# Optimization experiments

Hardware: AMD Instinct MI355X
Metric: run time of the kernel (lower is better)

## Reference

```python
import jax, jax.numpy as jnp
import numpy as np

B, D, NQ, NL, OUT = 256, 512, 16, 4, 10
NSTATES = 2 ** NQ
C64 = jnp.complex64


def _rx(t):
    c = jnp.cos(t / 2).astype(C64)
    s = (-1j * jnp.sin(t / 2)).astype(C64)
    return jnp.stack([jnp.stack([c, s], -1), jnp.stack([s, c], -1)], -2)


def _ry(t):
    c = jnp.cos(t / 2).astype(C64)
    s = jnp.sin(t / 2).astype(C64)
    return jnp.stack([jnp.stack([c, -s], -1), jnp.stack([s, c], -1)], -2)


def _rz(t):
    em = jnp.exp(-0.5j * t.astype(jnp.float32)).astype(C64)
    ep = jnp.exp(0.5j * t.astype(jnp.float32)).astype(C64)
    z = jnp.zeros_like(em)
    return jnp.stack([jnp.stack([em, z], -1), jnp.stack([z, ep], -1)], -2)


def _apply_gate(state, U, q, n):
    # state: (B, 2^n); U: (2,2) shared or (B,2,2) per-sample; qubit q is MSB-first
    b = state.shape[0]
    st = state.reshape(b, 2 ** q, 2, 2 ** (n - q - 1))
    if U.ndim == 2:
        st = jnp.einsum('ij,bajc->baic', U, st)
    else:
        st = jnp.einsum('bij,bajc->baic', U, st)
    return st.reshape(b, -1)


def _signs_table(n):
    # signs[i, q] = +-1 spin of qubit q (MSB-first) in basis state i
    idx = np.arange(2 ** n, dtype=np.int64)
    bits = (idx[:, None] >> (n - 1 - np.arange(n))[None, :]) & 1
    return jnp.asarray(1.0 - 2.0 * bits, dtype=jnp.float32)


def setup_inputs() -> dict:
    key = jax.random.key(0)
    ks = jax.random.split(key, 8)
    return {
        'x': jax.random.normal(ks[0], (B, D), dtype=jnp.float32),
        'W_enc': jax.random.normal(ks[1], (D, NQ), dtype=jnp.float32) * 0.05,
        'b_enc': jnp.zeros((NQ,), dtype=jnp.float32),
        'theta': jax.random.normal(ks[2], (NL, NQ, 3), dtype=jnp.float32) * 0.1,
        'phi': jax.random.normal(ks[3], (NL, NQ), dtype=jnp.float32) * 0.1,
        'W1': jax.random.normal(ks[4], (NQ, 2 * NQ), dtype=jnp.float32) * 0.1,
        'b1': jnp.zeros((2 * NQ,), dtype=jnp.float32),
        'W2': jax.random.normal(ks[5], (2 * NQ, OUT), dtype=jnp.float32) * 0.1,
        'b2': jnp.zeros((OUT,), dtype=jnp.float32),
    }


def reference(x, W_enc, b_enc, theta, phi, W1, b1, W2, b2):
    n, L = NQ, NL
    signs = _signs_table(n)                      # (2^n, n)
    zz = signs * jnp.roll(signs, -1, axis=1)     # ring ZZ couplings (2^n, n)

    # 1) classical -> angle encoding
    angles = jnp.tanh(x @ W_enc + b_enc) * jnp.pi          # (B, n)

    # 2) statevector init |0...0>
    state = jnp.zeros((x.shape[0], NSTATES), dtype=C64).at[:, 0].set(1.0)

    # 3) per-sample RY encoding layer
    for q in range(n):
        state = _apply_gate(state, _ry(angles[:, q]), q, n)

    # 4) variational layers: RZ->RY->RX per qubit, then entangling ZZ ring (diagonal)
    for l in range(L):
        for q in range(n):
            U = _rx(theta[l, q, 0]) @ _ry(theta[l, q, 1]) @ _rz(theta[l, q, 2])
            state = _apply_gate(state, U, q, n)
        phase = jnp.exp(-0.5j * (zz @ phi[l]))             # (2^n,)
        state = state * phase[None, :].astype(C64)

    # 5) <Z_q> expectation values
    probs = jnp.abs(state) ** 2                            # (B, 2^n)
    z = probs @ signs                                      # (B, n)

    # 6) classical decoder (dropout inactive at eval)
    h = jax.nn.relu(z @ W1 + b1)
    return h @ W2 + b2
```

## Files before the change

kernel.cpp:

```cpp
#include <hip/hip_runtime.h>


struct c32 { float x, y; };

__device__ __forceinline__ c32 cmul(c32 a, c32 b) {
  return { a.x * b.x - a.y * b.y, a.x * b.y + a.y * b.x };
}
__device__ __forceinline__ c32 C32(float2 f) { return { f.x, f.y }; }
__device__ __forceinline__ float2 F2(c32 a) { return make_float2(a.x, a.y); }
__device__ __forceinline__ c32 csel(c32 a, c32 b, int s) {
  return { s ? b.x : a.x, s ? b.y : a.y };
}

__device__ __forceinline__ void gate2(c32 &a0, c32 &a1, const c32 u[4]) {
  c32 b0 = a0, b1 = a1;
  a0.x = u[0].x * b0.x - u[0].y * b0.y + u[1].x * b1.x - u[1].y * b1.y;
  a0.y = u[0].x * b0.y + u[0].y * b0.x + u[1].x * b1.y + u[1].y * b1.x;
  a1.x = u[2].x * b0.x - u[2].y * b0.y + u[3].x * b1.x - u[3].y * b1.y;
  a1.y = u[2].x * b0.y + u[2].y * b0.x + u[3].x * b1.y + u[3].y * b1.x;
}

template <int ST>
__device__ __forceinline__ void rgate(c32 *a, const c32 u[4]) {
#pragma unroll
  for (int p = 0; p < 4; p++) {
    int i0 = ((p & ~(ST - 1)) << 1) | (p & (ST - 1));
    gate2(a[i0], a[i0 + ST], u);
  }
}

__device__ __forceinline__ void xgate(c32 *a, const c32 u[4], int lb, int lane) {
  int hi = (lane >> lb) & 1;
  c32 ua = csel(u[0], u[3], hi);
  c32 ub = csel(u[1], u[2], hi);
  int mask = 1 << lb;
#pragma unroll
  for (int r = 0; r < 8; r++) {
    float px = __shfl_xor(a[r].x, mask, 64);
    float py = __shfl_xor(a[r].y, mask, 64);
    c32 o = a[r];
    a[r].x = ua.x * o.x - ua.y * o.y + ub.x * px - ub.y * py;
    a[r].y = ua.x * o.y + ua.y * o.x + ub.x * py + ub.y * px;
  }
}

__device__ __forceinline__ void loadU(const float2* __restrict__ Ug, int idx, c32 u[4]) {
#pragma unroll
  for (int k = 0; k < 4; k++) u[k] = C32(Ug[idx * 4 + k]);
}

__device__ __forceinline__ void make_u(float t0, float t1, float t2, c32 u[4]) {
  float cx = cosf(0.5f * t0), sx = sinf(0.5f * t0);
  float cy = cosf(0.5f * t1), sy = sinf(0.5f * t1);
  float cz = cosf(0.5f * t2), sz = sinf(0.5f * t2);
  c32 M00 = {  cx * cy, -sx * sy };
  c32 M01 = { -cx * sy, -sx * cy };
  c32 M10 = {  cx * sy, -sx * cy };
  c32 M11 = {  cx * cy,  sx * sy };
  c32 em = { cz, -sz }, ep = { cz, sz };
  u[0] = cmul(M00, em);
  u[1] = cmul(M01, ep);
  u[2] = cmul(M10, em);
  u[3] = cmul(M11, ep);
}


__global__ __launch_bounds__(256) void k_prep(const float* __restrict__ x,
                                              const float* __restrict__ W,
                                              const float* __restrict__ be,
                                              const float* __restrict__ theta,
                                              const float* __restrict__ phi,
                                              float2* __restrict__ vtab,
                                              float2* __restrict__ Ug,
                                              float2* __restrict__ qph) {
  int t = threadIdx.x;
  if (blockIdx.x < 256) {
    int b = blockIdx.x;
    int q = t & 15, part = t >> 4;
    const float* xr = x + b * 512;
    float s = 0.f;
#pragma unroll 8
    for (int k = 0; k < 32; k++) {
      int d = part * 32 + k;
      s += xr[d] * W[d * 16 + q];
    }
    __shared__ float red[256];
    red[part * 16 + q] = s;
    __syncthreads();
    for (int st = 8; st > 0; st >>= 1) {
      if (part < st) red[part * 16 + q] += red[(part + st) * 16 + q];
      __syncthreads();
    }
    if (t < 16) {
      float a = tanhf(red[t] + be[t]) * 3.14159265358979323846f;
      float ca = cosf(0.5f * a), sa = sinf(0.5f * a);
      c32 u[4];
      make_u(theta[t * 3 + 0], theta[t * 3 + 1], theta[t * 3 + 2], u);
      vtab[b * 32 + t * 2]     = make_float2(u[0].x * ca + u[1].x * sa,
                                             u[0].y * ca + u[1].y * sa);
      vtab[b * 32 + t * 2 + 1] = make_float2(u[2].x * ca + u[3].x * sa,
                                             u[2].y * ca + u[3].y * sa);
    }
  } else {
    int idx = (blockIdx.x - 256) * 256 + t;
    if (idx < 48) {
      int l = idx >> 4, qq = idx & 15;
      const float* th = theta + ((l + 1) * 16 + qq) * 3;
      c32 u[4];
      make_u(th[0], th[1], th[2], u);
#pragma unroll
      for (int k = 0; k < 4; k++) Ug[idx * 4 + k] = F2(u[k]);
    }
    int q = idx >> 11, l = (idx >> 9) & 3, i = idx & 511;
    float A = 0.f;
    for (int m = l + 1; m <= 8 - l; m++) {
      int j = (q + 4 - m) & 15;
      float wv = phi[l * 16 + j];
      int sg = ((i >> m) ^ (i >> (m - 1))) & 1;
      A += sg ? -wv : wv;
    }
    qph[idx] = make_float2(cosf(0.5f * A), -sinf(0.5f * A));
  }
}


__global__ __launch_bounds__(1024) void k_cone_decode(const float2* __restrict__ vtab,
                                                      const float2* __restrict__ Ug,
                                                      const float2* __restrict__ qph,
                                                      const float* __restrict__ W1,
                                                      const float* __restrict__ b1,
                                                      const float* __restrict__ W2,
                                                      const float* __restrict__ b2,
                                                      float* __restrict__ out) {
  int b = blockIdx.x;
  int tid = threadIdx.x;
  int q = tid >> 6, lane = tid & 63;

  c32 vv0[9], vv1[9];
  const float2* vt = vtab + b * 32;
#pragma unroll
  for (int m = 0; m < 9; m++) {
    int jj = (q + 4 - m) & 15;
    vv0[m] = C32(vt[jj * 2]);
    vv1[m] = C32(vt[jj * 2 + 1]);
  }

  c32 lp = csel(vv0[0], vv1[0], lane & 1);
  lp = cmul(lp, csel(vv0[1], vv1[1], (lane >> 1) & 1));
  lp = cmul(lp, csel(vv0[2], vv1[2], (lane >> 2) & 1));
  lp = cmul(lp, csel(vv0[6], vv1[6], (lane >> 3) & 1));
  lp = cmul(lp, csel(vv0[7], vv1[7], (lane >> 4) & 1));
  lp = cmul(lp, csel(vv0[8], vv1[8], (lane >> 5) & 1));

  c32 a[8];
#pragma unroll
  for (int r = 0; r < 8; r++) {
    c32 tt = cmul(((r & 1) ? vv1[3] : vv0[3]), (((r >> 1) & 1) ? vv1[4] : vv0[4]));
    tt = cmul(tt, (((r >> 2) & 1) ? vv1[5] : vv0[5]));
    a[r] = cmul(lp, tt);
  }

  const float2* ph = qph + q * 2048;
  int ibase = (lane & 7) | (((lane >> 3) & 7) << 6);

  c32 u[4];
#pragma unroll
  for (int r = 0; r < 8; r++) a[r] = cmul(a[r], C32(ph[ibase | (r << 3)]));
  loadU(Ug, 0 * 16 + ((q + 3) & 15), u); xgate(a, u, 1, lane);
  loadU(Ug, 0 * 16 + ((q + 2) & 15), u); xgate(a, u, 2, lane);
  loadU(Ug, 0 * 16 + ((q + 1) & 15), u); rgate<1>(a, u);
  loadU(Ug, 0 * 16 + ( q          ), u); rgate<2>(a, u);
  loadU(Ug, 0 * 16 + ((q - 1) & 15), u); rgate<4>(a, u);
  loadU(Ug, 0 * 16 + ((q - 2) & 15), u); xgate(a, u, 3, lane);
  loadU(Ug, 0 * 16 + ((q - 3) & 15), u); xgate(a, u, 4, lane);
#pragma unroll
  for (int r = 0; r < 8; r++) a[r] = cmul(a[r], C32(ph[512 | ibase | (r << 3)]));
  loadU(Ug, 1 * 16 + ((q + 2) & 15), u); xgate(a, u, 2, lane);
  loadU(Ug, 1 * 16 + ((q + 1) & 15), u); rgate<1>(a, u);
  loadU(Ug, 1 * 16 + ( q          ), u); rgate<2>(a, u);
  loadU(Ug, 1 * 16 + ((q - 1) & 15), u); rgate<4>(a, u);
  loadU(Ug, 1 * 16 + ((q - 2) & 15), u); xgate(a, u, 3, lane);
#pragma unroll
  for (int r = 0; r < 8; r++) a[r] = cmul(a[r], C32(ph[1024 | ibase | (r << 3)]));
  loadU(Ug, 2 * 16 + ((q + 1) & 15), u); rgate<1>(a, u);
  loadU(Ug, 2 * 16 + ( q          ), u); rgate<2>(a, u);
  loadU(Ug, 2 * 16 + ((q - 1) & 15), u); rgate<4>(a, u);
#pragma unroll
  for (int r = 0; r < 8; r++) a[r] = cmul(a[r], C32(ph[1536 | ibase | (r << 3)]));

  float z = 0.f;
#pragma unroll
  for (int r = 0; r < 8; r++) {
    float p = a[r].x * a[r].x + a[r].y * a[r].y;
    z += ((r >> 1) & 1) ? -p : p;
  }
#pragma unroll
  for (int off = 32; off > 0; off >>= 1) z += __shfl_xor(z, off, 64);

  __shared__ float zsh[16];
  __shared__ float hsh[32];
  if (lane == 0) zsh[q] = z;
  __syncthreads();
  if (tid < 32) {
    float hj = b1[tid];
#pragma unroll
    for (int qq = 0; qq < 16; qq++) hj += zsh[qq] * W1[qq * 32 + tid];
    hsh[tid] = fmaxf(hj, 0.f);
  }
  __syncthreads();
  if (tid < 10) {
    float o = b2[tid];
#pragma unroll
    for (int j = 0; j < 32; j++) o += hsh[j] * W2[j * 10 + tid];
    out[b * 10 + tid] = o;
  }
}


extern "C" void kernel_launch(void* const* d_in, const int* in_sizes, int n_in,
                              void* d_out, int out_size, void* d_ws, size_t ws_size,
                              hipStream_t stream) {
  const float* x     = (const float*)d_in[0];
  const float* Wenc  = (const float*)d_in[1];
  const float* benc  = (const float*)d_in[2];
  const float* theta = (const float*)d_in[3];
  const float* phi   = (const float*)d_in[4];
  const float* W1    = (const float*)d_in[5];
  const float* b1    = (const float*)d_in[6];
  const float* W2    = (const float*)d_in[7];
  const float* b2    = (const float*)d_in[8];
  float* out = (float*)d_out;

  char* w = (char*)d_ws;
  float2* vtab  = (float2*)(w);
  float2* Ugtab = (float2*)(w + 65536);
  float2* qph   = (float2*)(w + 69632);

  k_prep<<<384, 256, 0, stream>>>(x, Wenc, benc, theta, phi, vtab, Ugtab, qph);
  k_cone_decode<<<256, 1024, 0, stream>>>(vtab, Ugtab, qph, W1, b1, W2, b2, out);
}
```

Measured before the change: 83.31 us.

## Fuse prep and cone kernels into one, compute ZZ phases inline

Merges the encoder/prep kernel into the light-cone simulation kernel so each block computes its own encoding angles, gate matrices (into shared memory), and halved phi values, removing one launch and the global workspace round trip. The precomputed phase table is replaced by computing ZZ phase sums per amplitude from lane bits and using fast __cosf/__sinf. The cost is that each block redundantly rebuilds the 48 shared gate matrices and does extra trig per amplitude, and fast trig reduces accuracy slightly.

```diff
diff --git a/kernel.cpp b/kernel.cpp
--- a/kernel.cpp
+++ b/kernel.cpp
@@ -11,6 +11,7 @@
 __device__ __forceinline__ c32 csel(c32 a, c32 b, int s) {
   return { s ? b.x : a.x, s ? b.y : a.y };
 }
+__device__ __forceinline__ float fsgn(int s, float w) { return s ? -w : w; }
 
 __device__ __forceinline__ void gate2(c32 &a0, c32 &a1, const c32 u[4]) {
   c32 b0 = a0, b1 = a1;
@@ -44,7 +45,7 @@
   }
 }
 
-__device__ __forceinline__ void loadU(const float2* __restrict__ Ug, int idx, c32 u[4]) {
+__device__ __forceinline__ void loadU(const float2* Ug, int idx, c32 u[4]) {
 #pragma unroll
   for (int k = 0; k < 4; k++) u[k] = C32(Ug[idx * 4 + k]);
 }
@@ -64,93 +65,96 @@
   u[3] = cmul(M11, ep);
 }
 
-
-__global__ __launch_bounds__(256) void k_prep(const float* __restrict__ x,
+__device__ __forceinline__ void diag8(c32 *a, float L, float w3p, float w4,
+                                      float w5, float w6p) {
+#pragma unroll
+  for (int r = 0; r < 8; r++) {
+    int r0 = r & 1, r1 = (r >> 1) & 1, r2 = (r >> 2) & 1;
+    float A = L + (r0 ? -w3p : w3p) + ((r1 ^ r0) ? -w4 : w4)
+                + ((r2 ^ r1) ? -w5 : w5) + (r2 ? -w6p : w6p);
+    c32 p = { __cosf(A), -__sinf(A) };
+    a[r] = cmul(a[r], p);
+  }
+}
+
+
+__global__ __launch_bounds__(1024) void k_all(const float* __restrict__ x,
                                               const float* __restrict__ W,
                                               const float* __restrict__ be,
                                               const float* __restrict__ theta,
                                               const float* __restrict__ phi,
-                                              float2* __restrict__ vtab,
-                                              float2* __restrict__ Ug,
-                                              float2* __restrict__ qph) {
-  int t = threadIdx.x;
-  if (blockIdx.x < 256) {
-    int b = blockIdx.x;
-    int q = t & 15, part = t >> 4;
-    const float* xr = x + b * 512;
+                                              const float* __restrict__ W1,
+                                              const float* __restrict__ b1,
+                                              const float* __restrict__ W2,
+                                              const float* __restrict__ b2,
+                                              float* __restrict__ out) {
+  __shared__ float  red[256];
+  __shared__ float2 vsh[32];
+  __shared__ float2 ugsh[192];
+  __shared__ float  phish[64];
+  __shared__ float  zsh[16];
+  __shared__ float  hsh[32];
+
+  int tid = threadIdx.x, b = blockIdx.x;
+  int lane = tid & 63, wv = tid >> 6;
+
+  {
+    int q16 = tid & 15, part = tid >> 4;
+    const float* xr = x + (b << 9);
     float s = 0.f;
-#pragma unroll 8
-    for (int k = 0; k < 32; k++) {
-      int d = part * 32 + k;
-      s += xr[d] * W[d * 16 + q];
+#pragma unroll
+    for (int k = 0; k < 8; k++) {
+      int d = (part << 3) + k;
+      s += xr[d] * W[(d << 4) + q16];
     }
-    __shared__ float red[256];
-    red[part * 16 + q] = s;
-    __syncthreads();
-    for (int st = 8; st > 0; st >>= 1) {
-      if (part < st) red[part * 16 + q] += red[(part + st) * 16 + q];
-      __syncthreads();
-    }
-    if (t < 16) {
-      float a = tanhf(red[t] + be[t]) * 3.14159265358979323846f;
-      float ca = cosf(0.5f * a), sa = sinf(0.5f * a);
-      c32 u[4];
-      make_u(theta[t * 3 + 0], theta[t * 3 + 1], theta[t * 3 + 2], u);
-      vtab[b * 32 + t * 2]     = make_float2(u[0].x * ca + u[1].x * sa,
-                                             u[0].y * ca + u[1].y * sa);
-      vtab[b * 32 + t * 2 + 1] = make_float2(u[2].x * ca + u[3].x * sa,
-                                             u[2].y * ca + u[3].y * sa);
-    }
-  } else {
-    int idx = (blockIdx.x - 256) * 256 + t;
-    if (idx < 48) {
-      int l = idx >> 4, qq = idx & 15;
-      const float* th = theta + ((l + 1) * 16 + qq) * 3;
-      c32 u[4];
-      make_u(th[0], th[1], th[2], u);
-#pragma unroll
-      for (int k = 0; k < 4; k++) Ug[idx * 4 + k] = F2(u[k]);
-    }
-    int q = idx >> 11, l = (idx >> 9) & 3, i = idx & 511;
-    float A = 0.f;
-    for (int m = l + 1; m <= 8 - l; m++) {
-      int j = (q + 4 - m) & 15;
-      float wv = phi[l * 16 + j];
-      int sg = ((i >> m) ^ (i >> (m - 1))) & 1;
-      A += sg ? -wv : wv;
-    }
-    qph[idx] = make_float2(cosf(0.5f * A), -sinf(0.5f * A));
-  }
-}
-
-
-__global__ __launch_bounds__(1024) void k_cone_decode(const float2* __restrict__ vtab,
-                                                      const float2* __restrict__ Ug,
-                                                      const float2* __restrict__ qph,
-                                                      const float* __restrict__ W1,
-                                                      const float* __restrict__ b1,
-                                                      const float* __restrict__ W2,
-                                                      const float* __restrict__ b2,
-                                                      float* __restrict__ out) {
-  int b = blockIdx.x;
-  int tid = threadIdx.x;
-  int q = tid >> 6, lane = tid & 63;
+    s += __shfl_xor(s, 16, 64);
+    s += __shfl_xor(s, 32, 64);
+    if (lane < 16) red[wv * 16 + lane] = s;
+  }
+  if (tid >= 960 && tid < 1008) {
+    int gl = tid - 960, l = gl >> 4, qq = gl & 15;
+    const float* th = theta + (((l + 1) << 4) + qq) * 3;
+    c32 u[4];
+    make_u(th[0], th[1], th[2], u);
+#pragma unroll
+    for (int k = 0; k < 4; k++) ugsh[gl * 4 + k] = F2(u[k]);
+  } else if (tid >= 896 && tid < 960) {
+    phish[tid - 896] = 0.5f * phi[tid - 896];
+  }
+  __syncthreads();
+  if (tid < 16) {
+    float acc = 0.f;
+#pragma unroll
+    for (int w = 0; w < 16; w++) acc += red[w * 16 + tid];
+    float a = tanhf(acc + be[tid]) * 3.14159265358979323846f;
+    float ca = __cosf(0.5f * a), sa = __sinf(0.5f * a);
+    c32 u[4];
+    make_u(theta[tid * 3 + 0], theta[tid * 3 + 1], theta[tid * 3 + 2], u);
+    vsh[tid * 2]     = make_float2(u[0].x * ca + u[1].x * sa,
+                                   u[0].y * ca + u[1].y * sa);
+    vsh[tid * 2 + 1] = make_float2(u[2].x * ca + u[3].x * sa,
+                                   u[2].y * ca + u[3].y * sa);
+  }
+  __syncthreads();
+
+  int q = wv;
+  int lb0 = lane & 1, lb1 = (lane >> 1) & 1, lb2 = (lane >> 2) & 1;
+  int lb3 = (lane >> 3) & 1, lb4 = (lane >> 4) & 1, lb5 = (lane >> 5) & 1;
 
   c32 vv0[9], vv1[9];
-  const float2* vt = vtab + b * 32;
 #pragma unroll
   for (int m = 0; m < 9; m++) {
     int jj = (q + 4 - m) & 15;
-    vv0[m] = C32(vt[jj * 2]);
-    vv1[m] = C32(vt[jj * 2 + 1]);
-  }
-
-  c32 lp = csel(vv0[0], vv1[0], lane & 1);
-  lp = cmul(lp, csel(vv0[1], vv1[1], (lane >> 1) & 1));
-  lp = cmul(lp, csel(vv0[2], vv1[2], (lane >> 2) & 1));
-  lp = cmul(lp, csel(vv0[6], vv1[6], (lane >> 3) & 1));
-  lp = cmul(lp, csel(vv0[7], vv1[7], (lane >> 4) & 1));
-  lp = cmul(lp, csel(vv0[8], vv1[8], (lane >> 5) & 1));
+    vv0[m] = C32(vsh[jj * 2]);
+    vv1[m] = C32(vsh[jj * 2 + 1]);
+  }
+
+  c32 lp = csel(vv0[0], vv1[0], lb0);
+  lp = cmul(lp, csel(vv0[1], vv1[1], lb1));
+  lp = cmul(lp, csel(vv0[2], vv1[2], lb2));
+  lp = cmul(lp, csel(vv0[6], vv1[6], lb3));
+  lp = cmul(lp, csel(vv0[7], vv1[7], lb4));
+  lp = cmul(lp, csel(vv0[8], vv1[8], lb5));
 
   c32 a[8];
 #pragma unroll
@@ -160,33 +164,34 @@
     a[r] = cmul(lp, tt);
   }
 
-  const float2* ph = qph + q * 2048;
-  int ibase = (lane & 7) | (((lane >> 3) & 7) << 6);
+#define PHW(l, m) phish[(l) * 16 + ((q + 4 - (m)) & 15)]
 
   c32 u[4];
-#pragma unroll
-  for (int r = 0; r < 8; r++) a[r] = cmul(a[r], C32(ph[ibase | (r << 3)]));
-  loadU(Ug, 0 * 16 + ((q + 3) & 15), u); xgate(a, u, 1, lane);
-  loadU(Ug, 0 * 16 + ((q + 2) & 15), u); xgate(a, u, 2, lane);
-  loadU(Ug, 0 * 16 + ((q + 1) & 15), u); rgate<1>(a, u);
-  loadU(Ug, 0 * 16 + ( q          ), u); rgate<2>(a, u);
-  loadU(Ug, 0 * 16 + ((q - 1) & 15), u); rgate<4>(a, u);
-  loadU(Ug, 0 * 16 + ((q - 2) & 15), u); xgate(a, u, 3, lane);
-  loadU(Ug, 0 * 16 + ((q - 3) & 15), u); xgate(a, u, 4, lane);
-#pragma unroll
-  for (int r = 0; r < 8; r++) a[r] = cmul(a[r], C32(ph[512 | ibase | (r << 3)]));
-  loadU(Ug, 1 * 16 + ((q + 2) & 15), u); xgate(a, u, 2, lane);
-  loadU(Ug, 1 * 16 + ((q + 1) & 15), u); rgate<1>(a, u);
-  loadU(Ug, 1 * 16 + ( q          ), u); rgate<2>(a, u);
-  loadU(Ug, 1 * 16 + ((q - 1) & 15), u); rgate<4>(a, u);
-  loadU(Ug, 1 * 16 + ((q - 2) & 15), u); xgate(a, u, 3, lane);
-#pragma unroll
-  for (int r = 0; r < 8; r++) a[r] = cmul(a[r], C32(ph[1024 | ibase | (r << 3)]));
-  loadU(Ug, 2 * 16 + ((q + 1) & 15), u); rgate<1>(a, u);
-  loadU(Ug, 2 * 16 + ( q          ), u); rgate<2>(a, u);
-  loadU(Ug, 2 * 16 + ((q - 1) & 15), u); rgate<4>(a, u);
-#pragma unroll
-  for (int r = 0; r < 8; r++) a[r] = cmul(a[r], C32(ph[1536 | ibase | (r << 3)]));
+  {
+    float L = fsgn(lb1 ^ lb0, PHW(0, 1)) + fsgn(lb2 ^ lb1, PHW(0, 2))
+            + fsgn(lb4 ^ lb3, PHW(0, 7)) + fsgn(lb5 ^ lb4, PHW(0, 8));
+    diag8(a, L, fsgn(lb2, PHW(0, 3)), PHW(0, 4), PHW(0, 5), fsgn(lb3, PHW(0, 6)));
+  }
+  loadU(ugsh, 0 * 16 + ((q + 3) & 15), u); xgate(a, u, 1, lane);
+  loadU(ugsh, 0 * 16 + ((q + 2) & 15), u); xgate(a, u, 2, lane);
+  loadU(ugsh, 0 * 16 + ((q + 1) & 15), u); rgate<1>(a, u);
+  loadU(ugsh, 0 * 16 + ( q          ), u); rgate<2>(a, u);
+  loadU(ugsh, 0 * 16 + ((q - 1) & 15), u); rgate<4>(a, u);
+  loadU(ugsh, 0 * 16 + ((q - 2) & 15), u); xgate(a, u, 3, lane);
+  loadU(ugsh, 0 * 16 + ((q - 3) & 15), u); xgate(a, u, 4, lane);
+  {
+    float L = fsgn(lb2 ^ lb1, PHW(1, 2)) + fsgn(lb4 ^ lb3, PHW(1, 7));
+    diag8(a, L, fsgn(lb2, PHW(1, 3)), PHW(1, 4), PHW(1, 5), fsgn(lb3, PHW(1, 6)));
+  }
+  loadU(ugsh, 1 * 16 + ((q + 2) & 15), u); xgate(a, u, 2, lane);
+  loadU(ugsh, 1 * 16 + ((q + 1) & 15), u); rgate<1>(a, u);
+  loadU(ugsh, 1 * 16 + ( q          ), u); rgate<2>(a, u);
+  loadU(ugsh, 1 * 16 + ((q - 1) & 15), u); rgate<4>(a, u);
+  loadU(ugsh, 1 * 16 + ((q - 2) & 15), u); xgate(a, u, 3, lane);
+  diag8(a, 0.f, fsgn(lb2, PHW(2, 3)), PHW(2, 4), PHW(2, 5), fsgn(lb3, PHW(2, 6)));
+  loadU(ugsh, 2 * 16 + ((q + 1) & 15), u); rgate<1>(a, u);
+  loadU(ugsh, 2 * 16 + ( q          ), u); rgate<2>(a, u);
+  loadU(ugsh, 2 * 16 + ((q - 1) & 15), u); rgate<4>(a, u);
 
   float z = 0.f;
 #pragma unroll
@@ -196,11 +201,9 @@
   }
 #pragma unroll
   for (int off = 32; off > 0; off >>= 1) z += __shfl_xor(z, off, 64);
-
-  __shared__ float zsh[16];
-  __shared__ float hsh[32];
   if (lane == 0) zsh[q] = z;
   __syncthreads();
+
   if (tid < 32) {
     float hj = b1[tid];
 #pragma unroll
@@ -214,6 +217,7 @@
     for (int j = 0; j < 32; j++) o += hsh[j] * W2[j * 10 + tid];
     out[b * 10 + tid] = o;
   }
+#undef PHW
 }
 
 
@@ -231,11 +235,5 @@
   const float* b2    = (const float*)d_in[8];
   float* out = (float*)d_out;
 
-  char* w = (char*)d_ws;
-  float2* vtab  = (float2*)(w);
-  float2* Ugtab = (float2*)(w + 65536);
-  float2* qph   = (float2*)(w + 69632);
-
-  k_prep<<<384, 256, 0, stream>>>(x, Wenc, benc, theta, phi, vtab, Ugtab, qph);
-  k_cone_decode<<<256, 1024, 0, stream>>>(vtab, Ugtab, qph, W1, b1, W2, b2, out);
-}
+  k_all<<<256, 1024, 0, stream>>>(x, Wenc, benc, theta, phi, W1, b1, W2, b2, out);
+}
```

Result: faster. 80.96 us (-2.8%).
